# Performance work log

Hardware: AMD Instinct MI355X
Metric: run time of the kernel (lower is better)

## Reference

```python
import jax, jax.numpy as jnp
import numpy as np

B, T, S = 2, 1024, 2048            # batch, query len, cache size
D, N, KH, H = 4096, 32, 8, 128     # emb_dim, q heads, kv heads, head_dim
ROPE_THETA = 1000000
EPS = 1e-6
K_MASK = jnp.finfo(jnp.bfloat16).min


def _rms_norm(x, scale):
    dtype = x.dtype
    rms = jnp.sqrt(jnp.mean(x.astype(jnp.float32) ** 2, axis=-1, keepdims=True) + EPS)
    return (scale * x / rms).astype(dtype)


def _rope_sincos(positions, head_dim):
    fraction = jnp.arange(0, head_dim, 2, dtype=jnp.float32) / head_dim
    inv_freq = 1.0 / (ROPE_THETA ** fraction)
    sinusoid = jnp.einsum('BT,k->BTk', positions.astype(jnp.float32), inv_freq,
                          precision=jax.lax.Precision.HIGHEST)
    return jnp.sin(sinusoid), jnp.cos(sinusoid)


def _apply_rope(x, sin, cos):
    half = x.shape[-1] // 2
    x1, x2 = x[..., :half], x[..., half:]
    sin, cos = sin[:, :, None, :], cos[:, :, None, :]
    return jnp.concatenate([x1 * cos - x2 * sin, x2 * cos + x1 * sin], axis=-1).astype(x.dtype)


def setup_inputs() -> dict:
    key = jax.random.key(0)
    ks = jax.random.split(key, 8)
    std = 0.01  # nnx.initializers.normal() default stddev
    return {
        'x': jax.random.normal(ks[0], (B, T, D), dtype=jnp.float32),
        'wq': jax.random.normal(ks[1], (D, N, H), dtype=jnp.float32) * std,
        'wk': jax.random.normal(ks[2], (D, KH, H), dtype=jnp.float32) * std,
        'wv': jax.random.normal(ks[3], (D, KH, H), dtype=jnp.float32) * std,
        'wo': jax.random.normal(ks[4], (N, H, D), dtype=jnp.float32) * std,
        'q_scale': jnp.ones((H,), dtype=jnp.float32),
        'k_scale': jnp.ones((H,), dtype=jnp.float32),
        'k_cache': jnp.zeros((B, S, KH, H), dtype=jnp.float32),
        'v_cache': jnp.zeros((B, S, KH, H), dtype=jnp.float32),
        'segment_ids': jnp.ones((B, T), dtype=jnp.int32),
        'num_right_pads': 0,
    }


def reference(x, wq, wk, wv, wo, q_scale, k_scale, k_cache, v_cache, segment_ids, num_right_pads):
    b, t, _ = x.shape
    s = k_cache.shape[1]
    n, kh, h = wq.shape[1], wk.shape[1], wq.shape[2]
    cur_ind = 0  # empty cache (prefill)

    q = _rms_norm(jnp.einsum('BTD,DNH->BTNH', x, wq), q_scale)      # [B,T,N,H]
    key = _rms_norm(jnp.einsum('BSD,DKH->BSKH', x, wk), k_scale)    # [B,T,K,H]
    val = jnp.einsum('BSD,DKH->BSKH', x, wv)                         # [B,T,K,H]

    # start_ind < 0 initially -> count left pads from segment_ids
    start = jnp.sum(jnp.cumsum(segment_ids != 0, axis=-1) == 0, -1).astype(jnp.int32)
    first = jnp.argmax(segment_ids, axis=1)
    pos = jnp.where(segment_ids != 0, jnp.arange(t, dtype=jnp.int32) - first[:, None], 2 ** 30)
    position_ids = pos + cur_ind

    sin, cos = _rope_sincos(position_ids, h)
    q = _apply_rope(q, sin, cos)
    key = _apply_rope(key, sin, cos)

    k_cache = jax.lax.dynamic_update_slice(k_cache, key, (0, cur_ind, 0, 0))
    v_cache = jax.lax.dynamic_update_slice(v_cache, val, (0, cur_ind, 0, 0))

    g = n // kh
    qr = q.reshape(b, t, kh, g, h)
    logits = jnp.einsum('BTHGD,BSHD->BHGTS', qr, k_cache) * (h ** -0.5)

    q_pos = cur_ind + jnp.arange(t, dtype=jnp.int32)[None, :] - start[:, None]
    ts = jnp.arange(s, dtype=jnp.int32)
    kv_seg = ((ts[None, :] >= start[:, None]) & (ts[None, :] < cur_ind + t)).astype(segment_ids.dtype)
    k_pos = ts[None, :] - start[:, None]
    causal = k_pos[:, None, :] <= q_pos[:, :, None]                  # [B,T,S]
    seg_mask = kv_seg[:, None, :] == segment_ids[:, :, None]        # [B,T,S]
    mask = causal & seg_mask

    logits = jnp.where(mask[:, None, None, :, :], logits, K_MASK)
    w = jax.nn.softmax(logits.astype(jnp.float32), axis=-1).astype(logits.dtype)
    qkv = jnp.einsum('BHGTS,BSHD->BTHGD', w, v_cache).reshape(b, t, n, h)
    return jnp.einsum('BTNH,NHD->BTD', qkv, wo)
```

## Files before the change

kernel.cpp:

```cpp
#include <hip/hip_runtime.h>

constexpr int Bc  = 2;
constexpr int Tc  = 1024;
constexpr int Dc  = 4096;
constexpr int NHc = 32;
constexpr int KHc = 8;
constexpr int Hc  = 128;

typedef __bf16 bf16;
typedef bf16  bf16x4  __attribute__((ext_vector_type(4)));
typedef bf16  bf16x8  __attribute__((ext_vector_type(8)));
typedef float floatx4 __attribute__((ext_vector_type(4)));

#define MFMA16(a, b, c) __builtin_amdgcn_mfma_f32_16x16x32_bf16((a), (b), (c), 0, 0, 0)

__device__ __forceinline__ void gload_lds16(const bf16* g, bf16* l) {
    __builtin_amdgcn_global_load_lds(
        (const __attribute__((address_space(1))) void*)g,
        (__attribute__((address_space(3))) void*)l, 16, 0, 0);
}

__global__ void seg_scan(const int* __restrict__ seg, int* __restrict__ start) {
    int b = threadIdx.x;
    if (b >= Bc) return;
    int f = 0;
    for (int t = 0; t < Tc; ++t) {
        if (seg[b * Tc + t] != 0) { f = t; break; }
    }
    start[b] = f;
}

__global__ __launch_bounds__(256) void cvt_f32_bf16(const float* __restrict__ in,
                                                    bf16* __restrict__ out) {
    const size_t i = ((size_t)blockIdx.x * 256 + threadIdx.x) * 8;
    float4 f0 = *(const float4*)(in + i);
    float4 f1 = *(const float4*)(in + i + 4);
    bf16x8 v;
    v[0] = (bf16)f0.x; v[1] = (bf16)f0.y; v[2] = (bf16)f0.z; v[3] = (bf16)f0.w;
    v[4] = (bf16)f1.x; v[5] = (bf16)f1.y; v[6] = (bf16)f1.z; v[7] = (bf16)f1.w;
    *(bf16x8*)(out + i) = v;
}

__global__ __launch_bounds__(256) void transpose_cvt(const float* __restrict__ in,
                                                     bf16* __restrict__ out,
                                                     int R, int C) {
    __shared__ float tile[64][65];
    const int c0 = blockIdx.x * 64, r0 = blockIdx.y * 64;
    const int tx = threadIdx.x & 15, ty = threadIdx.x >> 4;
#pragma unroll
    for (int i = 0; i < 4; ++i) {
        float4 f = *(const float4*)&in[(size_t)(r0 + ty * 4 + i) * C + c0 + tx * 4];
        tile[ty * 4 + i][tx * 4 + 0] = f.x;
        tile[ty * 4 + i][tx * 4 + 1] = f.y;
        tile[ty * 4 + i][tx * 4 + 2] = f.z;
        tile[ty * 4 + i][tx * 4 + 3] = f.w;
    }
    __syncthreads();
#pragma unroll
    for (int i = 0; i < 4; ++i) {
        const int cc = ty * 4 + i;
        bf16x4 v;
        v[0] = (bf16)tile[tx * 4 + 0][cc];
        v[1] = (bf16)tile[tx * 4 + 1][cc];
        v[2] = (bf16)tile[tx * 4 + 2][cc];
        v[3] = (bf16)tile[tx * 4 + 3][cc];
        *(bf16x4*)&out[(size_t)(c0 + cc) * R + r0 + tx * 4] = v;
    }
}

__global__ __launch_bounds__(256) void v_transpose(const bf16* __restrict__ src,
                                                   bf16* __restrict__ dst,
                                                   int srcstride) {
    __shared__ bf16 tl[32][136];
    const int bk = blockIdx.y;
    const int b = bk / KHc, kh = bk % KHc;
    const int t0 = blockIdx.x * 32;
    const int tid = threadIdx.x;
    {
        const int j = tid >> 3;
        const int c = tid & 7;
        const bf16* p = src + (size_t)(b * Tc + t0 + j) * srcstride + kh * Hc + c * 16;
        *(bf16x8*)&tl[j][c * 16]     = *(const bf16x8*)p;
        *(bf16x8*)&tl[j][c * 16 + 8] = *(const bf16x8*)(p + 8);
    }
    __syncthreads();
    {
        const int d = tid >> 1;
        const int toff = (tid & 1) * 16;
        bf16x8 v0, v1;
#pragma unroll
        for (int k = 0; k < 8; ++k) v0[k] = tl[toff + k][d];
#pragma unroll
        for (int k = 0; k < 8; ++k) v1[k] = tl[toff + 8 + k][d];
        bf16* o = dst + ((size_t)bk * Hc + d) * Tc + t0 + toff;
        *(bf16x8*)o       = v0;
        *(bf16x8*)(o + 8) = v1;
    }
}

template <typename OT>
__global__ __launch_bounds__(256) void gemm128(const bf16* __restrict__ A,
                                               const bf16* __restrict__ Bt,
                                               OT* __restrict__ C,
                                               int M, int K, int N) {
    __shared__ alignas(16) bf16 As[128 * 32];
    __shared__ alignas(16) bf16 Bs[128 * 32];
    const int m0 = blockIdx.y * 128, n0 = blockIdx.x * 128;
    const int tid = threadIdx.x;
    const int w = tid >> 6, L = tid & 63, quad = L >> 4, lid = L & 15;
    const int wm = (w & 1) * 64, wn = (w >> 1) * 64;

    const int srow = w * 32 + (L >> 2);
    const int chk  = (L & 3) ^ ((L >> 3) & 3);
    const bf16* gA = A  + (size_t)(m0 + srow) * K + chk * 8;
    const bf16* gB = Bt + (size_t)(n0 + srow) * K + chk * 8;
    bf16* lA0 = &As[(w * 32) * 32];
    bf16* lA1 = &As[(w * 32 + 16) * 32];
    bf16* lB0 = &Bs[(w * 32) * 32];
    bf16* lB1 = &Bs[(w * 32 + 16) * 32];

    const bf16* ap[4]; const bf16* bp[4];
#pragma unroll
    for (int i = 0; i < 4; ++i) {
        const int ra = wm + i * 16 + lid;
        ap[i] = &As[ra * 32 + (quad ^ ((ra >> 1) & 3)) * 8];
        const int rb = wn + i * 16 + lid;
        bp[i] = &Bs[rb * 32 + (quad ^ ((rb >> 1) & 3)) * 8];
    }

    floatx4 acc[4][4] = {};

    for (int k0 = 0; k0 < K; k0 += 32) {
        __syncthreads();
        gload_lds16(gA + k0,                  lA0);
        gload_lds16(gA + (size_t)16 * K + k0, lA1);
        gload_lds16(gB + k0,                  lB0);
        gload_lds16(gB + (size_t)16 * K + k0, lB1);
        __syncthreads();

        bf16x8 af[4], bfr[4];
#pragma unroll
        for (int i = 0; i < 4; ++i) af[i]  = *(const bf16x8*)ap[i];
#pragma unroll
        for (int j = 0; j < 4; ++j) bfr[j] = *(const bf16x8*)bp[j];
#pragma unroll
        for (int i = 0; i < 4; ++i)
#pragma unroll
            for (int j = 0; j < 4; ++j)
                acc[i][j] = MFMA16(af[i], bfr[j], acc[i][j]);
    }

#pragma unroll
    for (int i = 0; i < 4; ++i) {
#pragma unroll
        for (int r = 0; r < 4; ++r) {
            const size_t row = (size_t)(m0 + wm + i * 16 + quad * 4 + r);
#pragma unroll
            for (int j = 0; j < 4; ++j)
                C[row * N + (n0 + wn + j * 16 + lid)] = (OT)acc[i][j][r];
        }
    }
}

__global__ __launch_bounds__(256) void rms_rope(bf16* __restrict__ buf,
                                                const float* __restrict__ scale,
                                                const int* __restrict__ start,
                                                int nheads, int rowstride) {
    const int gid = blockIdx.x * 4 + (threadIdx.x >> 6);
    const int L   = threadIdx.x & 63;
    const int h   = gid % nheads;
    const int t   = (gid / nheads) % Tc;
    const int b   = gid / (nheads * Tc);
    bf16* p = buf + (size_t)(b * Tc + t) * rowstride + h * Hc;

    float x1 = (float)p[L], x2 = (float)p[L + 64];
    float ss = x1 * x1 + x2 * x2;
#pragma unroll
    for (int off = 1; off < 64; off <<= 1) ss += __shfl_xor(ss, off);
    const float inv = 1.f / sqrtf(ss * (1.0f / 128.0f) + 1e-6f);
    const float y1 = scale[L] * x1 * inv;
    const float y2 = scale[L + 64] * x2 * inv;

    const int   pos = t - start[b];
    const float fr  = (float)L * (1.0f / 64.0f);
    const float invf = exp2f(-19.9315686f * fr);
    const float ang = (float)pos * invf;
    float sn, cs;
    sincosf(ang, &sn, &cs);

    p[L]      = (bf16)(y1 * cs - y2 * sn);
    p[L + 64] = (bf16)(y2 * cs + y1 * sn);
}

__global__ __launch_bounds__(256) void attn_kernel(const bf16* __restrict__ q,
                                                   const bf16* __restrict__ k,
                                                   const bf16* __restrict__ vt,
                                                   bf16* __restrict__ outp,
                                                   const int* __restrict__ start,
                                                   int qstride, int kstride) {
    __shared__ alignas(16) bf16 Ks[32 * 128];
    __shared__ alignas(16) bf16 VT[128 * 32];
    __shared__ alignas(16) bf16 pS[4][16][40];

    const int tblk = blockIdx.x, n = blockIdx.y, b = blockIdx.z;
    const int kh   = n >> 2;
    const int tid  = threadIdx.x, w = tid >> 6, L = tid & 63;
    const int quad = L >> 4, lid = L & 15;
    const int t0   = tblk * 64 + w * 16;
    const int st   = start[b];

    const bf16* qrow = q + (size_t)(b * Tc + t0 + lid) * qstride + n * Hc;
    bf16x8 aqf[4];
#pragma unroll
    for (int c = 0; c < 4; ++c) aqf[c] = *(const bf16x8*)(qrow + c * 32 + quad * 8);

    const int kr0 = w * 8 + (L >> 4);
    const int kr1 = kr0 + 4;
    const bf16* gK0 = k + (size_t)(b * Tc + kr0) * kstride + kh * Hc
                        + (((L & 15) ^ (kr0 & 15)) * 8);
    const bf16* gK1 = k + (size_t)(b * Tc + kr1) * kstride + kh * Hc
                        + (((L & 15) ^ (kr1 & 15)) * 8);
    bf16* lK0 = &Ks[(w * 8) * 128];
    bf16* lK1 = &Ks[(w * 8 + 4) * 128];

    const int vd0 = (w * 2) * 16 + (L >> 2);
    const int vd1 = vd0 + 16;
    const bf16* vbase = vt + (size_t)((b * KHc + kh) * Hc) * Tc;
    const bf16* gV0 = vbase + (size_t)vd0 * Tc + (((L & 3) ^ (vd0 & 3) ^ ((vd0 >> 2) & 3)) * 8);
    const bf16* gV1 = vbase + (size_t)vd1 * Tc + (((L & 3) ^ (vd1 & 3) ^ ((vd1 >> 2) & 3)) * 8);
    bf16* lV0 = &VT[(w * 2) * 512];
    bf16* lV1 = &VT[(w * 2 + 1) * 512];

    const bf16* kf[4][2];
#pragma unroll
    for (int c = 0; c < 4; ++c) {
        kf[c][0] = &Ks[lid * 128        + (((c * 4 + quad) ^ lid) * 8)];
        kf[c][1] = &Ks[(16 + lid) * 128 + (((c * 4 + quad) ^ lid) * 8)];
    }
    const int vpos = (quad ^ (lid & 3) ^ ((lid >> 2) & 3)) * 8;
    const bf16* vf[8];
#pragma unroll
    for (int cg = 0; cg < 8; ++cg) vf[cg] = &VT[(cg * 16 + lid) * 32 + vpos];

    floatx4 oacc[8] = {};
    float lsum[4] = {0.f, 0.f, 0.f, 0.f};
    const int sEnd = tblk * 64 + 64;

    for (int s0 = 0; s0 < sEnd; s0 += 32) {
        __syncthreads();
        gload_lds16(gK0 + (size_t)s0 * kstride, lK0);
        gload_lds16(gK1 + (size_t)s0 * kstride, lK1);
        gload_lds16(gV0 + s0, lV0);
        gload_lds16(gV1 + s0, lV1);
        __syncthreads();

        floatx4 sc0 = {0.f, 0.f, 0.f, 0.f}, sc1 = {0.f, 0.f, 0.f, 0.f};
#pragma unroll
        for (int c = 0; c < 4; ++c) {
            sc0 = MFMA16(aqf[c], *(const bf16x8*)kf[c][0], sc0);
            sc1 = MFMA16(aqf[c], *(const bf16x8*)kf[c][1], sc1);
        }

#pragma unroll
        for (int r = 0; r < 4; ++r) {
            const int tq  = t0 + quad * 4 + r;
            const int sk0 = s0 + lid, sk1 = s0 + 16 + lid;
            const float p0 = (sk0 <= tq && sk0 >= st)
                               ? __expf(sc0[r] * 0.08838834764831845f - 16.f) : 0.f;
            const float p1 = (sk1 <= tq && sk1 >= st)
                               ? __expf(sc1[r] * 0.08838834764831845f - 16.f) : 0.f;
            lsum[r] += p0 + p1;
            pS[w][quad * 4 + r][lid]      = (bf16)p0;
            pS[w][quad * 4 + r][16 + lid] = (bf16)p1;
        }
        asm volatile("s_waitcnt lgkmcnt(0)" ::: "memory");

        bf16x8 pa = *(const bf16x8*)&pS[w][lid][quad * 8];
#pragma unroll
        for (int cg = 0; cg < 8; ++cg)
            oacc[cg] = MFMA16(pa, *(const bf16x8*)vf[cg], oacc[cg]);
    }

#pragma unroll
    for (int r = 0; r < 4; ++r) {
        lsum[r] += __shfl_xor(lsum[r], 1);
        lsum[r] += __shfl_xor(lsum[r], 2);
        lsum[r] += __shfl_xor(lsum[r], 4);
        lsum[r] += __shfl_xor(lsum[r], 8);
    }

#pragma unroll
    for (int cg = 0; cg < 8; ++cg) {
#pragma unroll
        for (int r = 0; r < 4; ++r) {
            const int t = t0 + quad * 4 + r;
            outp[((size_t)(b * Tc + t) * NHc + n) * Hc + cg * 16 + lid] =
                (bf16)(oacc[cg][r] / lsum[r]);
        }
    }
}

extern "C" void kernel_launch(void* const* d_in, const int* in_sizes, int n_in,
                              void* d_out, int out_size, void* d_ws, size_t ws_size,
                              hipStream_t stream) {
    const float* x       = (const float*)d_in[0];
    const float* wq      = (const float*)d_in[1];
    const float* wk      = (const float*)d_in[2];
    const float* wv      = (const float*)d_in[3];
    const float* wo      = (const float*)d_in[4];
    const float* q_scale = (const float*)d_in[5];
    const float* k_scale = (const float*)d_in[6];
    const int*   seg     = (const int*)d_in[9];
    float*       out     = (float*)d_out;

    char* ws = (char*)d_ws;
    bf16* wcomb = (bf16*)(ws);
    bf16* vtb   = (bf16*)(ws + (32ull << 20));
    bf16* qkvb  = (bf16*)(ws + (48ull << 20));
    bf16* xb    = (bf16*)(ws + (72ull << 20));
    bf16* ab    = xb;
    int*  stb   = (int*) (ws + (88ull << 20));

    seg_scan<<<1, 64, 0, stream>>>(seg, stb);

    cvt_f32_bf16<<<(Bc * Tc * Dc) / (256 * 8), 256, 0, stream>>>(x, xb);

    transpose_cvt<<<dim3(64, 64), 256, 0, stream>>>(wq, wcomb, Dc, NHc * Hc);
    transpose_cvt<<<dim3(16, 64), 256, 0, stream>>>(wk, wcomb + (size_t)4096 * Dc, Dc, KHc * Hc);
    transpose_cvt<<<dim3(16, 64), 256, 0, stream>>>(wv, wcomb + (size_t)5120 * Dc, Dc, KHc * Hc);

    gemm128<bf16><<<dim3(48, 16), 256, 0, stream>>>(xb, wcomb, qkvb,
                                                    Bc * Tc, Dc, 6144);

    rms_rope<<<(Bc * Tc * NHc) / 4, 256, 0, stream>>>(qkvb, q_scale, stb, NHc, 6144);
    rms_rope<<<(Bc * Tc * KHc) / 4, 256, 0, stream>>>(qkvb + 4096, k_scale, stb, KHc, 6144);

    v_transpose<<<dim3(Tc / 32, Bc * KHc), 256, 0, stream>>>(qkvb + 5120, vtb, 6144);

    transpose_cvt<<<dim3(64, 64), 256, 0, stream>>>(wo, wcomb, NHc * Hc, Dc);

    attn_kernel<<<dim3(Tc / 64, NHc, Bc), 256, 0, stream>>>(
        qkvb, qkvb + 4096, vtb, ab, stb, 6144, 6144);

    gemm128<float><<<dim3(32, 16), 256, 0, stream>>>(ab, wcomb, out,
                                                     Bc * Tc, NHc * Hc, Dc);
}
```

Before: 543.1 us.

## Replace QKV projection GEMM with 256x256-tile four-stage LDS ring pipeline

Adds a new GEMM kernel with 256x256 output tiles, 512 threads and a four-deep ring of LDS buffers filled by direct global-to-LDS loads with XOR swizzling. It is used for the fused QKV projection in place of the 128-tile GEMM. The aim is more reuse of each loaded tile and hiding of global load latency behind MFMA work. In exchange it uses a large LDS footprint (128 KB per block) and more accumulator registers. The grid drops to 192 blocks, which may underfill the GPU's compute units.

```diff
diff --git a/kernel.cpp b/kernel.cpp
--- a/kernel.cpp
+++ b/kernel.cpp
@@ -162,6 +162,96 @@
     }
 }
 
+template <typename OT>
+__global__ __launch_bounds__(512, 2) void gemm_ring256(const bf16* __restrict__ A,
+                                                       const bf16* __restrict__ Bt,
+                                                       OT* __restrict__ C,
+                                                       int M, int K, int N) {
+    __shared__ alignas(16) bf16 ring[4][16384];
+    const int m0 = blockIdx.y * 256, n0 = blockIdx.x * 256;
+    const int tid = threadIdx.x;
+    const int w = tid >> 6, L = tid & 63, quad = L >> 4, lid = L & 15;
+    const int wr = w >> 2, wc = w & 3;
+
+    const int srow = tid >> 2;
+    const int schk = ((tid & 3) ^ ((tid >> 3) & 3)) * 8;
+    const bf16* gA0 = A  + (size_t)(m0 + srow) * K + schk;
+    const bf16* gA1 = A  + (size_t)(m0 + 128 + srow) * K + schk;
+    const bf16* gB0 = Bt + (size_t)(n0 + srow) * K + schk;
+    const bf16* gB1 = Bt + (size_t)(n0 + 128 + srow) * K + schk;
+    const int ldsA0 = (w * 16) * 32;
+    const int ldsA1 = (128 + w * 16) * 32;
+    const int ldsB0 = 8192 + (w * 16) * 32;
+    const int ldsB1 = 8192 + (128 + w * 16) * 32;
+
+    int offA[8], offB[4];
+#pragma unroll
+    for (int m = 0; m < 8; ++m) {
+        const int row = wr * 128 + m * 16 + lid;
+        offA[m] = row * 32 + ((quad ^ ((row >> 1) & 3)) * 8);
+    }
+#pragma unroll
+    for (int n = 0; n < 4; ++n) {
+        const int row = wc * 64 + n * 16 + lid;
+        offB[n] = 8192 + row * 32 + ((quad ^ ((row >> 1) & 3)) * 8);
+    }
+
+    const int NT = K >> 5;
+
+    auto stage = [&](int kt) {
+        bf16* sb = ring[kt & 3];
+        const size_t ko = (size_t)kt << 5;
+        gload_lds16(gA0 + ko, sb + ldsA0);
+        gload_lds16(gA1 + ko, sb + ldsA1);
+        gload_lds16(gB0 + ko, sb + ldsB0);
+        gload_lds16(gB1 + ko, sb + ldsB1);
+    };
+
+    stage(0); stage(1); stage(2);
+    asm volatile("s_waitcnt vmcnt(8)" ::: "memory");
+    __builtin_amdgcn_s_barrier();
+    __builtin_amdgcn_sched_barrier(0);
+
+    floatx4 acc[8][4] = {};
+
+    for (int t = 0; t < NT; ++t) {
+        int ts = t + 3; if (ts >= NT) ts -= NT;
+        stage(ts);
+
+        const bf16* sb = ring[t & 3];
+        bf16x8 af[8], bfr[4];
+#pragma unroll
+        for (int m = 0; m < 8; ++m) af[m]  = *(const bf16x8*)(sb + offA[m]);
+#pragma unroll
+        for (int n = 0; n < 4; ++n) bfr[n] = *(const bf16x8*)(sb + offB[n]);
+
+        __builtin_amdgcn_s_setprio(1);
+#pragma unroll
+        for (int m = 0; m < 8; ++m)
+#pragma unroll
+            for (int n = 0; n < 4; ++n)
+                acc[m][n] = MFMA16(af[m], bfr[n], acc[m][n]);
+        __builtin_amdgcn_s_setprio(0);
+
+        asm volatile("s_waitcnt vmcnt(8)" ::: "memory");
+        __builtin_amdgcn_s_barrier();
+        __builtin_amdgcn_sched_barrier(0);
+    }
+
+    asm volatile("s_waitcnt vmcnt(0)" ::: "memory");
+
+#pragma unroll
+    for (int m = 0; m < 8; ++m) {
+#pragma unroll
+        for (int r = 0; r < 4; ++r) {
+            const size_t row = (size_t)(m0 + wr * 128 + m * 16 + quad * 4 + r);
+#pragma unroll
+            for (int n = 0; n < 4; ++n)
+                C[row * N + (n0 + wc * 64 + n * 16 + lid)] = (OT)acc[m][n][r];
+        }
+    }
+}
+
 __global__ __launch_bounds__(256) void rms_rope(bf16* __restrict__ buf,
                                                 const float* __restrict__ scale,
                                                 const int* __restrict__ start,
@@ -329,8 +419,8 @@
     transpose_cvt<<<dim3(16, 64), 256, 0, stream>>>(wk, wcomb + (size_t)4096 * Dc, Dc, KHc * Hc);
     transpose_cvt<<<dim3(16, 64), 256, 0, stream>>>(wv, wcomb + (size_t)5120 * Dc, Dc, KHc * Hc);
 
-    gemm128<bf16><<<dim3(48, 16), 256, 0, stream>>>(xb, wcomb, qkvb,
-                                                    Bc * Tc, Dc, 6144);
+    gemm_ring256<bf16><<<dim3(24, 8), 512, 0, stream>>>(xb, wcomb, qkvb,
+                                                        Bc * Tc, Dc, 6144);
 
     rms_rope<<<(Bc * Tc * NHc) / 4, 256, 0, stream>>>(qkvb, q_scale, stb, NHc, 6144);
     rms_rope<<<(Bc * Tc * KHc) / 4, 256, 0, stream>>>(qkvb + 4096, k_scale, stb, KHc, 6144);
```

After: 530.3 us. -2.4%, faster.

## Use 128x192 tiled GEMM with triple-buffered LDS ring for QKV projection

Applied to the files above, without the earlier changes.

Adds a new GEMM kernel for the fused QKV projection. It uses 128x192 output tiles, so the grid has 512 blocks instead of 768. It also uses a three-slot LDS ring that prefetches two K-steps ahead through direct global-to-LDS loads, with a single barrier per iteration. MFMA issue priority is raised during compute. The aim is to hide load latency better and raise arithmetic intensity per block, at the cost of more registers and LDS. The wraparound prefetch issues redundant loads on the last two iterations.

```diff
diff --git a/kernel.cpp b/kernel.cpp
--- a/kernel.cpp
+++ b/kernel.cpp
@@ -162,6 +162,100 @@
     }
 }
 
+template <typename OT>
+__global__ __launch_bounds__(256, 2) void gemm_ring192(const bf16* __restrict__ A,
+                                                       const bf16* __restrict__ Bt,
+                                                       OT* __restrict__ C,
+                                                       int M, int K, int N) {
+    __shared__ alignas(16) bf16 ring[3][10240];
+    const int m0 = blockIdx.y * 128, n0 = blockIdx.x * 192;
+    const int tid = threadIdx.x;
+    const int w = tid >> 6, L = tid & 63, quad = L >> 4, lid = L & 15;
+    const int wr = w >> 1, wc = w & 1;
+
+    const int srow = tid >> 2;
+    const int schk = ((tid & 3) ^ ((tid >> 3) & 3)) * 8;
+    const bf16* gA = A  + (size_t)(m0 + srow) * K + schk;
+    const bf16* gB = Bt + (size_t)(n0 + srow) * K + schk;
+    const size_t K64 = (size_t)64 * K, K128 = (size_t)128 * K;
+    const int ldsA0 = (w * 16) * 32;
+    const int ldsA1 = (64 + w * 16) * 32;
+    const int ldsB0 = 4096 + (w * 16) * 32;
+    const int ldsB1 = 4096 + (64 + w * 16) * 32;
+    const int ldsB2 = 4096 + (128 + w * 16) * 32;
+
+    int offA[4], offB[6];
+#pragma unroll
+    for (int m = 0; m < 4; ++m) {
+        const int row = wr * 64 + m * 16 + lid;
+        offA[m] = row * 32 + ((quad ^ ((row >> 1) & 3)) * 8);
+    }
+#pragma unroll
+    for (int n = 0; n < 6; ++n) {
+        const int row = wc * 96 + n * 16 + lid;
+        offB[n] = 4096 + row * 32 + ((quad ^ ((row >> 1) & 3)) * 8);
+    }
+
+    const int NT = K >> 5;
+
+    auto stage = [&](int kt, int sl) {
+        bf16* sb = ring[sl];
+        const size_t ko = (size_t)kt << 5;
+        gload_lds16(gA + ko,         sb + ldsA0);
+        gload_lds16(gA + K64 + ko,   sb + ldsA1);
+        gload_lds16(gB + ko,         sb + ldsB0);
+        gload_lds16(gB + K64 + ko,   sb + ldsB1);
+        gload_lds16(gB + K128 + ko,  sb + ldsB2);
+    };
+
+    stage(0, 0); stage(1, 1);
+    asm volatile("s_waitcnt vmcnt(5)" ::: "memory");
+    __builtin_amdgcn_s_barrier();
+    __builtin_amdgcn_sched_barrier(0);
+
+    floatx4 acc[4][6] = {};
+    int cur = 0;
+
+    for (int t = 0; t < NT; ++t) {
+        int ts = t + 2; if (ts >= NT) ts -= NT;
+        int ss = cur + 2; if (ss >= 3) ss -= 3;
+        stage(ts, ss);
+
+        const bf16* sb = ring[cur];
+        bf16x8 af[4], bfr[6];
+#pragma unroll
+        for (int m = 0; m < 4; ++m) af[m]  = *(const bf16x8*)(sb + offA[m]);
+#pragma unroll
+        for (int n = 0; n < 6; ++n) bfr[n] = *(const bf16x8*)(sb + offB[n]);
+
+        __builtin_amdgcn_s_setprio(1);
+#pragma unroll
+        for (int m = 0; m < 4; ++m)
+#pragma unroll
+            for (int n = 0; n < 6; ++n)
+                acc[m][n] = MFMA16(af[m], bfr[n], acc[m][n]);
+        __builtin_amdgcn_s_setprio(0);
+
+        asm volatile("s_waitcnt vmcnt(5)" ::: "memory");
+        __builtin_amdgcn_s_barrier();
+        __builtin_amdgcn_sched_barrier(0);
+        cur = (cur == 2) ? 0 : cur + 1;
+    }
+
+    asm volatile("s_waitcnt vmcnt(0)" ::: "memory");
+
+#pragma unroll
+    for (int m = 0; m < 4; ++m) {
+#pragma unroll
+        for (int r = 0; r < 4; ++r) {
+            const size_t row = (size_t)(m0 + wr * 64 + m * 16 + quad * 4 + r);
+#pragma unroll
+            for (int n = 0; n < 6; ++n)
+                C[row * N + (n0 + wc * 96 + n * 16 + lid)] = (OT)acc[m][n][r];
+        }
+    }
+}
+
 __global__ __launch_bounds__(256) void rms_rope(bf16* __restrict__ buf,
                                                 const float* __restrict__ scale,
                                                 const int* __restrict__ start,
@@ -329,8 +423,8 @@
     transpose_cvt<<<dim3(16, 64), 256, 0, stream>>>(wk, wcomb + (size_t)4096 * Dc, Dc, KHc * Hc);
     transpose_cvt<<<dim3(16, 64), 256, 0, stream>>>(wv, wcomb + (size_t)5120 * Dc, Dc, KHc * Hc);
 
-    gemm128<bf16><<<dim3(48, 16), 256, 0, stream>>>(xb, wcomb, qkvb,
-                                                    Bc * Tc, Dc, 6144);
+    gemm_ring192<bf16><<<dim3(32, 16), 256, 0, stream>>>(xb, wcomb, qkvb,
+                                                         Bc * Tc, Dc, 6144);
 
     rms_rope<<<(Bc * Tc * NHc) / 4, 256, 0, stream>>>(qkvb, q_scale, stb, NHc, 6144);
     rms_rope<<<(Bc * Tc * KHc) / 4, 256, 0, stream>>>(qkvb + 4096, k_scale, stb, KHc, 6144);
```

After: 520.7 us. 1.04x faster.
